# Kernel optimization log

Measured on AMD Instinct MI355X. Metric: run time of the kernel, lower is better.

## Reference

```python
import jax, jax.numpy as jnp
import numpy as np

V, E, H, K, B, T = 50000, 256, 512, 12, 32, 256
START, STOP = 10, 11
NEG = -10000.0
Hd = H // 2


def _lstm(x, h0, c0, Wih, Whh, bih, bhh):
    # x: [T, B, D] -> hidden states [T, B, Hd]; PyTorch gate order i,f,g,o
    def step(carry, xt):
        h, c = carry
        g = xt @ Wih.T + bih + h @ Whh.T + bhh
        i, f, gg, o = jnp.split(g, 4, axis=-1)
        c = jax.nn.sigmoid(f) * c + jax.nn.sigmoid(i) * jnp.tanh(gg)
        h = jax.nn.sigmoid(o) * jnp.tanh(c)
        return (h, c), h
    _, hs = jax.lax.scan(step, (h0, c0), x)
    return hs


def setup_inputs() -> dict:
    key = jax.random.key(0)
    ks = jax.random.split(key, 12)
    inp = {}
    inp["sentence"] = jax.random.randint(ks[0], (B, T), 0, V, dtype=jnp.int32)
    lens = jax.random.randint(ks[1], (B,), 1, T + 1, dtype=jnp.int32)
    inp["seq_lens"] = jnp.sort(lens)[::-1]  # pack_padded requires descending
    emb = jax.random.normal(ks[2], (V, E)) * 0.05
    inp["emb"] = emb.at[0].set(0.0)  # padding_idx=0
    def lw(k):
        a, b, c, d = jax.random.split(k, 4)
        return (jax.random.normal(a, (4 * Hd, E)) * 0.05,
                jax.random.normal(b, (4 * Hd, Hd)) * 0.05,
                jax.random.normal(c, (4 * Hd,)) * 0.05,
                jax.random.normal(d, (4 * Hd,)) * 0.05)
    inp["Wih_f"], inp["Whh_f"], inp["bih_f"], inp["bhh_f"] = lw(ks[3])
    inp["Wih_b"], inp["Whh_b"], inp["bih_b"], inp["bhh_b"] = lw(ks[4])
    inp["h0"] = jax.random.normal(ks[5], (2, B, Hd))  # init_hidden uses randn
    inp["c0"] = jax.random.normal(ks[6], (2, B, Hd))
    inp["W_out"] = jax.random.normal(ks[7], (K, H)) * 0.05
    inp["b_out"] = jax.random.normal(ks[8], (K,)) * 0.05
    trans = jax.random.normal(ks[9], (K, K))
    inp["transitions"] = trans.at[START, :].set(NEG).at[:, STOP].set(NEG)
    return inp


def _features(sentence, seq_lens, emb, Wih_f, Whh_f, bih_f, bhh_f,
              Wih_b, Whh_b, bih_b, bhh_b, h0, c0, W_out, b_out):
    x = emb[sentence]                       # [B,T,E]
    t_idx = jnp.arange(T)
    # forward direction
    hf = _lstm(x.transpose(1, 0, 2), h0[0], c0[0], Wih_f, Whh_f, bih_f, bhh_f)
    hf = hf.transpose(1, 0, 2)              # [B,T,Hd]
    # backward direction: reverse each sequence within its length (packed semantics)
    rev_idx = jnp.where(t_idx[None, :] < seq_lens[:, None],
                        seq_lens[:, None] - 1 - t_idx[None, :], t_idx[None, :])  # [B,T]
    x_rev = jnp.take_along_axis(x, rev_idx[:, :, None], axis=1)
    hb_rev = _lstm(x_rev.transpose(1, 0, 2), h0[1], c0[1], Wih_b, Whh_b, bih_b, bhh_b)
    hb = jnp.take_along_axis(hb_rev.transpose(1, 0, 2), rev_idx[:, :, None], axis=1)
    hcat = jnp.concatenate([hf, hb], axis=-1)  # [B,T,H]
    return hcat @ W_out.T + b_out              # [B,T,K]


def _viterbi(feats, seq_lens, transitions):
    t_idx = jnp.arange(T)
    mask = t_idx[None, :] < seq_lens[:, None]           # [B,T]
    init = jnp.full((B, K), NEG).at[:, START].set(0.0)  # forward_var

    def vstep(fv, inputs):
        feat_t, m_t = inputs                            # [B,K], [B]
        scores = fv[:, None, :] + transitions[None, :, :]   # [B, next, prev]
        bp = jnp.argmax(scores, axis=-1)                # [B,K]
        best = jnp.max(scores, axis=-1) + feat_t
        return jnp.where(m_t[:, None], best, fv), bp

    fv, bps = jax.lax.scan(vstep, init, (feats.transpose(1, 0, 2), mask.T))
    terminal = fv + transitions[STOP][None, :]          # [B,K]
    best_last = jnp.argmax(terminal, axis=-1)           # [B]
    path_scores = jnp.take_along_axis(terminal, best_last[:, None], axis=1)[:, 0]

    def btstep(tag, inputs):
        bp_t, m_t = inputs
        pred_t = jnp.where(m_t, tag, -1)
        prev = jnp.take_along_axis(bp_t, tag[:, None], axis=1)[:, 0]
        return jnp.where(m_t, prev, tag), pred_t

    _, preds_rev = jax.lax.scan(btstep, best_last, (bps[::-1], mask.T[::-1]))
    preds = preds_rev[::-1].transpose(1, 0)             # [B,T], -1 past seq_len
    return path_scores, preds


def reference(sentence, seq_lens, emb, Wih_f, Whh_f, bih_f, bhh_f,
              Wih_b, Whh_b, bih_b, bhh_b, h0, c0, W_out, b_out, transitions):
    feats = _features(sentence, seq_lens, emb, Wih_f, Whh_f, bih_f, bhh_f,
                      Wih_b, Whh_b, bih_b, bhh_b, h0, c0, W_out, b_out)
    scores, preds = _viterbi(feats, seq_lens, transitions)
    return scores, preds
```

## Files before the change

### kernel.cpp

```cpp
#include <hip/hip_runtime.h>
#include <math.h>

#define T_ 256
#define B_ 32
#define E_ 256
#define HD_ 256
#define NG_ 1024
#define K_ 12
#define START_ 10
#define STOP_ 11
#define NEG_ -10000.0f
#define MAGICU 0x40000000u

typedef float f4_t __attribute__((ext_vector_type(4)));

__device__ __forceinline__ float sigf(float x) { return 1.0f / (1.0f + expf(-x)); }

__global__ void tok_gather(const int* __restrict__ sent, const int* __restrict__ lens,
                           int* __restrict__ tokA) {
    int e = blockIdx.x * 256 + threadIdx.x;
    int dir = e >> 13, m = e & 8191, t = m >> 5, b = m & 31;
    int len = lens[b];
    int tt = dir ? (t < len ? len - 1 - t : t) : t;
    tokA[e] = sent[b * T_ + tt];
}

__global__ void whh_tr(const float* __restrict__ Wf, const float* __restrict__ Wb,
                       float* __restrict__ WT) {
    int dir = blockIdx.x >> 8, k = blockIdx.x & 255, u = threadIdx.x;
    const float* W = dir ? Wb : Wf;
    float4 v;
    v.x = W[(0 * HD_ + u) * HD_ + k];
    v.y = W[(1 * HD_ + u) * HD_ + k];
    v.z = W[(2 * HD_ + u) * HD_ + k];
    v.w = W[(3 * HD_ + u) * HD_ + k];
    ((float4*)(WT + ((size_t)dir * 256 + k) * NG_))[u] = v;
}

__global__ void hex_init(float* __restrict__ hex) {
    int i = blockIdx.x * 256 + threadIdx.x;
    float4 m = make_float4(2.0f, 2.0f, 2.0f, 2.0f);
    ((float4*)hex)[i] = m;
}

__global__ __launch_bounds__(256) void in_gemm(
    const float* __restrict__ emb, const int* __restrict__ tokA,
    const float* __restrict__ Wih_f, const float* __restrict__ Wih_b,
    const float* __restrict__ bih_f, const float* __restrict__ bhh_f,
    const float* __restrict__ bih_b, const float* __restrict__ bhh_b,
    float* __restrict__ G) {
    const int dir = blockIdx.z;
    const int n0 = blockIdx.x * 128, m0 = blockIdx.y * 128;
    const float* Wih = dir ? Wih_b : Wih_f;
    const float* bihp = dir ? bih_b : bih_f;
    const float* bhhp = dir ? bhh_b : bhh_f;
    __shared__ float As[8][128];
    __shared__ float Bs[8][128];
    const int tid = threadIdx.x;
    const int rs = tid >> 1, kc = (tid & 1) * 4;
    const int tok = tokA[dir * 8192 + m0 + rs];
    const float* arow = emb + (size_t)tok * E_;
    const int np = n0 + rs;
    const int wrow = ((np & 3) << 8) | (np >> 2);
    const float* brow = Wih + (size_t)wrow * E_;
    const int ty = tid >> 4, tx = tid & 15;

    float acc[8][8];
#pragma unroll
    for (int i = 0; i < 8; ++i)
#pragma unroll
        for (int j = 0; j < 8; ++j) acc[i][j] = 0.f;

    for (int k0 = 0; k0 < E_; k0 += 8) {
        float4 av = *(const float4*)(arow + k0 + kc);
        float4 bv = *(const float4*)(brow + k0 + kc);
        __syncthreads();
        As[kc + 0][rs] = av.x; As[kc + 1][rs] = av.y; As[kc + 2][rs] = av.z; As[kc + 3][rs] = av.w;
        Bs[kc + 0][rs] = bv.x; Bs[kc + 1][rs] = bv.y; Bs[kc + 2][rs] = bv.z; Bs[kc + 3][rs] = bv.w;
        __syncthreads();
#pragma unroll
        for (int k = 0; k < 8; ++k) {
            float4 a0 = *(const float4*)&As[k][ty * 8];
            float4 a1 = *(const float4*)&As[k][ty * 8 + 4];
            float4 b0 = *(const float4*)&Bs[k][tx * 8];
            float4 b1 = *(const float4*)&Bs[k][tx * 8 + 4];
            float af8[8] = {a0.x, a0.y, a0.z, a0.w, a1.x, a1.y, a1.z, a1.w};
            float bf8[8] = {b0.x, b0.y, b0.z, b0.w, b1.x, b1.y, b1.z, b1.w};
#pragma unroll
            for (int i = 0; i < 8; ++i)
#pragma unroll
                for (int j = 0; j < 8; ++j) acc[i][j] += af8[i] * bf8[j];
        }
    }
    float bias[8];
#pragma unroll
    for (int j = 0; j < 8; ++j) {
        int nn = n0 + tx * 8 + j;
        int wr = ((nn & 3) << 8) | (nn >> 2);
        bias[j] = bihp[wr] + bhhp[wr];
    }
#pragma unroll
    for (int i = 0; i < 8; ++i) {
        int m = m0 + ty * 8 + i;
        float* gp = G + ((size_t)dir * 8192 + m) * NG_ + n0 + tx * 8;
        float4 o0 = {acc[i][0] + bias[0], acc[i][1] + bias[1], acc[i][2] + bias[2], acc[i][3] + bias[3]};
        float4 o1 = {acc[i][4] + bias[4], acc[i][5] + bias[5], acc[i][6] + bias[6], acc[i][7] + bias[7]};
        *(float4*)gp = o0;
        *(float4*)(gp + 4) = o1;
    }
}

__global__ __launch_bounds__(512, 2) void lstm_rec8(
    const float* __restrict__ WhhT, const float* __restrict__ G,
    const float* __restrict__ h0, const float* __restrict__ c0,
    const int* __restrict__ lens, float* __restrict__ hex) {
    const int wg = blockIdx.x;
    const int dir = wg >> 5, bt = (wg >> 3) & 3, ut = wg & 7;
    const int tid = threadIdx.x;
    const int wv = tid >> 6, ln = tid & 63;
    const int upair = ln & 15;
    const int kssub = ln >> 4;
    const int ksup = wv >> 1, bh = wv & 1;
    const int ks = ksup * 4 + kssub;
    const int sb = bh * 4 + (ln & 3);
    const int sk = ksup * 64 + (ln >> 2) * 4;
    const int speer = sk >> 5;

    __shared__ float4 hsA4[256];
    __shared__ float4 hsB4[256];
    __shared__ float4 red4[512 * 11];
    __shared__ float4 hT4[64];

    const int Tmax = lens[bt * 8];

    const float4* WT4 = (const float4*)(WhhT + (size_t)dir * 256 * NG_);
    const int gu_e = ut * 32 + upair * 2;
    float4 We[16], Wo[16];
#pragma unroll
    for (int j = 0; j < 16; ++j) {
        We[j] = WT4[(ks * 16 + j) * 256 + gu_e];
        Wo[j] = WT4[(ks * 16 + j) * 256 + gu_e + 1];
    }

    const bool is_act = (ln < 32);
    float c = 0.f;
    float4 gpend = make_float4(0.f, 0.f, 0.f, 0.f);
    const float* Gd = G + (size_t)dir * 8192 * NG_;
    if (is_act) {
        c = c0[(dir * B_ + bt * 8 + wv) * HD_ + ut * 32 + ln];
        gpend = ((const float4*)(Gd + (size_t)(bt * 8 + wv) * NG_))[ut * 32 + ln];
    }

    float* hexg = hex + (size_t)(dir * 4 + bt) * T_ * 2048;
    float4* hsX4 = bh ? hsB4 : hsA4;
    float* hsX = (float*)hsX4;

    f4_t pend;

    for (int t = 0; t < Tmax; ++t) {
        float4 hv;
        if (t == 0) {
            hv = *(const float4*)(h0 + (size_t)(dir * B_ + bt * 8 + sb) * HD_ + sk);
        } else if (speer == ut) {
            hv = hT4[sb * 8 + ((sk & 31) >> 2)];
        } else {
            asm volatile("s_waitcnt vmcnt(0)" ::: "memory");
            hv.x = pend.x; hv.y = pend.y; hv.z = pend.z; hv.w = pend.w;
            if (__float_as_uint(hv.x) == MAGICU || __float_as_uint(hv.y) == MAGICU ||
                __float_as_uint(hv.z) == MAGICU || __float_as_uint(hv.w) == MAGICU) {
                const float* src = hexg + (size_t)(t - 1) * 2048 + sb * 256 + sk;
                int it = 0;
                for (;;) {
                    __builtin_amdgcn_s_sleep(1);
                    float a0 = __hip_atomic_load(src + 0, __ATOMIC_RELAXED, __HIP_MEMORY_SCOPE_AGENT);
                    float a1 = __hip_atomic_load(src + 1, __ATOMIC_RELAXED, __HIP_MEMORY_SCOPE_AGENT);
                    float a2 = __hip_atomic_load(src + 2, __ATOMIC_RELAXED, __HIP_MEMORY_SCOPE_AGENT);
                    float a3 = __hip_atomic_load(src + 3, __ATOMIC_RELAXED, __HIP_MEMORY_SCOPE_AGENT);
                    if (!(__float_as_uint(a0) == MAGICU || __float_as_uint(a1) == MAGICU ||
                          __float_as_uint(a2) == MAGICU || __float_as_uint(a3) == MAGICU)) {
                        hv = make_float4(a0, a1, a2, a3); break;
                    }
                    if (++it > (1 << 22)) break;
                }
            }
        }
        hsX[(sk + 0) * 4 + (ln & 3)] = hv.x;
        hsX[(sk + 1) * 4 + (ln & 3)] = hv.y;
        hsX[(sk + 2) * 4 + (ln & 3)] = hv.z;
        hsX[(sk + 3) * 4 + (ln & 3)] = hv.w;
        asm volatile("s_waitcnt lgkmcnt(0)" ::: "memory");

        float4 ae0 = {0,0,0,0}, ae1 = {0,0,0,0}, ae2 = {0,0,0,0}, ae3 = {0,0,0,0};
        float4 ao0 = {0,0,0,0}, ao1 = {0,0,0,0}, ao2 = {0,0,0,0}, ao3 = {0,0,0,0};
#pragma unroll
        for (int j = 0; j < 16; ++j) {
            float4 h4 = hsX4[ks * 16 + j];
            float4 we = We[j], wo = Wo[j];
            ae0.x += we.x*h4.x; ae0.y += we.y*h4.x; ae0.z += we.z*h4.x; ae0.w += we.w*h4.x;
            ae1.x += we.x*h4.y; ae1.y += we.y*h4.y; ae1.z += we.z*h4.y; ae1.w += we.w*h4.y;
            ae2.x += we.x*h4.z; ae2.y += we.y*h4.z; ae2.z += we.z*h4.z; ae2.w += we.w*h4.z;
            ae3.x += we.x*h4.w; ae3.y += we.y*h4.w; ae3.z += we.z*h4.w; ae3.w += we.w*h4.w;
            ao0.x += wo.x*h4.x; ao0.y += wo.y*h4.x; ao0.z += wo.z*h4.x; ao0.w += wo.w*h4.x;
            ao1.x += wo.x*h4.y; ao1.y += wo.y*h4.y; ao1.z += wo.z*h4.y; ao1.w += wo.w*h4.y;
            ao2.x += wo.x*h4.z; ao2.y += wo.y*h4.z; ao2.z += wo.z*h4.z; ao2.w += wo.w*h4.z;
            ao3.x += wo.x*h4.w; ao3.y += wo.y*h4.w; ao3.z += wo.z*h4.w; ao3.w += wo.w*h4.w;
        }
        {
            float4* r = &red4[((wv * 4 + kssub) * 16 + upair) * 11 + kssub];
            r[0] = ae0; r[1] = ae1; r[2] = ae2; r[3] = ae3;
            r[4] = ao0; r[5] = ao1; r[6] = ao2; r[7] = ao3;
        }
        asm volatile("s_waitcnt lgkmcnt(0)\n\ts_barrier" ::: "memory");

        if (is_act) {
            const int b = wv, u = ln;
            const int bhv = b >> 2, bq = b & 3, up = u >> 1, par = u & 1;
            float si = gpend.x, sf = gpend.y, sg = gpend.z, so = gpend.w;
#pragma unroll
            for (int kq = 0; kq < 4; ++kq)
#pragma unroll
                for (int kr = 0; kr < 4; ++kr) {
                    float4 p = red4[(((kq * 2 + bhv) * 4 + kr) * 16 + up) * 11 + kr + par * 4 + bq];
                    si += p.x; sf += p.y; sg += p.z; so += p.w;
                }
            c = sigf(sf) * c + sigf(si) * tanhf(sg);
            float h = sigf(so) * tanhf(c);
            ((float*)hT4)[b * 32 + u] = h;
            float* dst = hexg + (size_t)t * 2048 + b * 256 + ut * 32 + u;
            asm volatile("global_store_dword %0, %1, off sc0 sc1" :: "v"(dst), "v"(h) : "memory");
            if (t + 1 < Tmax)
                gpend = ((const float4*)(Gd + ((size_t)(t + 1) * B_ + bt * 8 + b) * NG_))[ut * 32 + u];
        }
        if (t + 1 < Tmax && speer != ut) {
            const float* nsrc = hexg + (size_t)t * 2048 + sb * 256 + sk;
            asm volatile("global_load_dwordx4 %0, %1, off sc0 sc1"
                         : "=v"(pend) : "v"(nsrc) : "memory");
        }
        asm volatile("s_waitcnt lgkmcnt(0)\n\ts_barrier" ::: "memory");
    }
}

__global__ void feat_k(const float* __restrict__ hex, const int* __restrict__ lens,
                       const float* __restrict__ Wout, const float* __restrict__ bout,
                       float* __restrict__ feats) {
    int tid = threadIdx.x;
    int pl = tid / 12, k = tid % 12;
    int p = blockIdx.x * 16 + pl;
    int b = p >> 8, t = p & 255;
    int len = lens[b];
    int tr = t < len ? len - 1 - t : t;
    const float4* hf = (const float4*)(hex + ((size_t)(b >> 3) * T_ + t) * 2048 + (b & 7) * 256);
    const float4* hb = (const float4*)(hex + ((size_t)(4 + (b >> 3)) * T_ + tr) * 2048 + (b & 7) * 256);
    const float4* w0 = (const float4*)(Wout + (size_t)k * 512);
    const float4* w1 = (const float4*)(Wout + (size_t)k * 512 + 256);
    float acc = bout[k];
#pragma unroll 4
    for (int j = 0; j < 64; ++j) {
        float4 h4 = hf[j], v4 = w0[j];
        acc += h4.x * v4.x + h4.y * v4.y + h4.z * v4.z + h4.w * v4.w;
    }
#pragma unroll 4
    for (int j = 0; j < 64; ++j) {
        float4 h4 = hb[j], v4 = w1[j];
        acc += h4.x * v4.x + h4.y * v4.y + h4.z * v4.z + h4.w * v4.w;
    }
    feats[(size_t)p * K_ + k] = acc;
}

__global__ __launch_bounds__(512) void viterbi_k(
    const float* __restrict__ feats, const float* __restrict__ trans,
    const int* __restrict__ lens, float* __restrict__ out) {
    __shared__ float fv[2][B_][16];
    __shared__ float tl[K_][16];
    __shared__ unsigned char bp[T_][B_][6];
    __shared__ int best_last[B_];
    int tid = threadIdx.x;
    int b = tid >> 4, lane = tid & 15;
    if (tid < K_ * K_) tl[tid / 12][tid % 12] = trans[tid];
    if (lane < K_) fv[0][b][lane] = (lane == START_) ? 0.f : NEG_;
    __syncthreads();
    int len = lens[b];
    int pp = 0;
    float f_cur = 0.f;
    if (lane < K_) f_cur = feats[(size_t)b * T_ * K_ + lane];
    for (int t = 0; t < T_; ++t) {
        float f_nxt = 0.f;
        if (t + 1 < T_ && lane < K_) f_nxt = feats[((size_t)b * T_ + t + 1) * K_ + lane];
        if (lane < K_) {
            float best = fv[pp][b][0] + tl[lane][0];
            int argp = 0;
#pragma unroll
            for (int p = 1; p < K_; ++p) {
                float v = fv[pp][b][p] + tl[lane][p];
                if (v > best) { best = v; argp = p; }
            }
            float nb = best + f_cur;
            fv[pp ^ 1][b][lane] = (t < len) ? nb : fv[pp][b][lane];
            int other = __shfl_xor(argp, 1);
            if ((lane & 1) == 0) bp[t][b][lane >> 1] = (unsigned char)(argp | (other << 4));
        }
        __syncthreads();
        pp ^= 1;
        f_cur = f_nxt;
    }
    if (lane == 0) {
        float best = fv[pp][b][0] + tl[STOP_][0];
        int bl = 0;
#pragma unroll
        for (int p = 1; p < K_; ++p) {
            float v = fv[pp][b][p] + tl[STOP_][p];
            if (v > best) { best = v; bl = p; }
        }
        out[b] = best;
        best_last[b] = bl;
    }
    __syncthreads();
    if (lane == 0) {
        int tag = best_last[b];
        for (int t = T_ - 1; t >= 0; --t) {
            int m = (t < len);
            out[B_ + b * T_ + t] = (float)(m ? tag : -1);
            if (m) tag = (bp[t][b][tag >> 1] >> ((tag & 1) * 4)) & 15;
        }
    }
}

extern "C" void kernel_launch(void* const* d_in, const int* in_sizes, int n_in,
                              void* d_out, int out_size, void* d_ws, size_t ws_size,
                              hipStream_t stream) {
    const int*   sent  = (const int*)d_in[0];
    const int*   lens  = (const int*)d_in[1];
    const float* emb   = (const float*)d_in[2];
    const float* Wih_f = (const float*)d_in[3];
    const float* Whh_f = (const float*)d_in[4];
    const float* bih_f = (const float*)d_in[5];
    const float* bhh_f = (const float*)d_in[6];
    const float* Wih_b = (const float*)d_in[7];
    const float* Whh_b = (const float*)d_in[8];
    const float* bih_b = (const float*)d_in[9];
    const float* bhh_b = (const float*)d_in[10];
    const float* h0    = (const float*)d_in[11];
    const float* c0    = (const float*)d_in[12];
    const float* Wout  = (const float*)d_in[13];
    const float* bout  = (const float*)d_in[14];
    const float* trans = (const float*)d_in[15];
    float* out = (float*)d_out;

    char* ws = (char*)d_ws;
    int*   tokA  = (int*)ws;
    float* WhhT  = (float*)(ws + 65536);
    float* G     = (float*)(ws + 2162688);
    float* feats = (float*)(ws + 69271552);
    float* hex   = (float*)(ws + 69664768);

    tok_gather<<<64, 256, 0, stream>>>(sent, lens, tokA);
    whh_tr<<<512, 256, 0, stream>>>(Whh_f, Whh_b, WhhT);
    hex_init<<<4096, 256, 0, stream>>>(hex);
    in_gemm<<<dim3(8, 64, 2), 256, 0, stream>>>(emb, tokA, Wih_f, Wih_b,
                                                bih_f, bhh_f, bih_b, bhh_b, G);
    lstm_rec8<<<64, 512, 0, stream>>>(WhhT, G, h0, c0, lens, hex);
    feat_k<<<512, 192, 0, stream>>>(hex, lens, Wout, bout, feats);
    viterbi_k<<<1, 512, 0, stream>>>(feats, trans, lens, out);
}
```

Measured before the change: 1.132 ms.

## Remap recurrence blocks across XCDs and relax coherence bits on peer hidden-state loads

The block-to-work mapping changes so the 8 blocks that share a direction and batch tile (exchanging h each step) get consecutive-by-8 block IDs. With round-robin dispatch these likely land on the same XCD and share its L2. Peer h loads drop the sc1 bit, and the spin loop uses a vector load that only bypasses further every fourth try. This aims to cut cross-die coherence latency on each step's h exchange, but it relies on co-location and could read stale data or spin longer if blocks land on different XCDs.

```diff
diff --git a/kernel.cpp b/kernel.cpp
--- a/kernel.cpp
+++ b/kernel.cpp
@@ -110,12 +110,13 @@
     }
 }
 
-__global__ __launch_bounds__(512, 2) void lstm_rec8(
+__global__ __launch_bounds__(512, 2) void lstm_rec9(
     const float* __restrict__ WhhT, const float* __restrict__ G,
     const float* __restrict__ h0, const float* __restrict__ c0,
     const int* __restrict__ lens, float* __restrict__ hex) {
-    const int wg = blockIdx.x;
-    const int dir = wg >> 5, bt = (wg >> 3) & 3, ut = wg & 7;
+    const int g = blockIdx.x & 7;
+    const int ut = blockIdx.x >> 3;
+    const int dir = g >> 2, bt = g & 3;
     const int tid = threadIdx.x;
     const int wv = tid >> 6, ln = tid & 63;
     const int upair = ln & 15;
@@ -152,8 +153,6 @@
     }
 
     float* hexg = hex + (size_t)(dir * 4 + bt) * T_ * 2048;
-    float4* hsX4 = bh ? hsB4 : hsA4;
-    float* hsX = (float*)hsX4;
 
     f4_t pend;
 
@@ -172,24 +171,30 @@
                 int it = 0;
                 for (;;) {
                     __builtin_amdgcn_s_sleep(1);
-                    float a0 = __hip_atomic_load(src + 0, __ATOMIC_RELAXED, __HIP_MEMORY_SCOPE_AGENT);
-                    float a1 = __hip_atomic_load(src + 1, __ATOMIC_RELAXED, __HIP_MEMORY_SCOPE_AGENT);
-                    float a2 = __hip_atomic_load(src + 2, __ATOMIC_RELAXED, __HIP_MEMORY_SCOPE_AGENT);
-                    float a3 = __hip_atomic_load(src + 3, __ATOMIC_RELAXED, __HIP_MEMORY_SCOPE_AGENT);
-                    if (!(__float_as_uint(a0) == MAGICU || __float_as_uint(a1) == MAGICU ||
-                          __float_as_uint(a2) == MAGICU || __float_as_uint(a3) == MAGICU)) {
-                        hv = make_float4(a0, a1, a2, a3); break;
+                    f4_t r;
+                    if ((it & 3) == 3) {
+                        asm volatile("global_load_dwordx4 %0, %1, off sc0 sc1\n\ts_waitcnt vmcnt(0)"
+                                     : "=v"(r) : "v"(src) : "memory");
+                    } else {
+                        asm volatile("global_load_dwordx4 %0, %1, off sc0\n\ts_waitcnt vmcnt(0)"
+                                     : "=v"(r) : "v"(src) : "memory");
+                    }
+                    if (!(__float_as_uint(r.x) == MAGICU || __float_as_uint(r.y) == MAGICU ||
+                          __float_as_uint(r.z) == MAGICU || __float_as_uint(r.w) == MAGICU)) {
+                        hv.x = r.x; hv.y = r.y; hv.z = r.z; hv.w = r.w; break;
                     }
                     if (++it > (1 << 22)) break;
                 }
             }
         }
+        float* hsX = (float*)(bh ? hsB4 : hsA4);
         hsX[(sk + 0) * 4 + (ln & 3)] = hv.x;
         hsX[(sk + 1) * 4 + (ln & 3)] = hv.y;
         hsX[(sk + 2) * 4 + (ln & 3)] = hv.z;
         hsX[(sk + 3) * 4 + (ln & 3)] = hv.w;
         asm volatile("s_waitcnt lgkmcnt(0)" ::: "memory");
 
+        const float4* hsX4 = bh ? hsB4 : hsA4;
         float4 ae0 = {0,0,0,0}, ae1 = {0,0,0,0}, ae2 = {0,0,0,0}, ae3 = {0,0,0,0};
         float4 ao0 = {0,0,0,0}, ao1 = {0,0,0,0}, ao2 = {0,0,0,0}, ao3 = {0,0,0,0};
 #pragma unroll
@@ -233,7 +238,7 @@
         }
         if (t + 1 < Tmax && speer != ut) {
             const float* nsrc = hexg + (size_t)t * 2048 + sb * 256 + sk;
-            asm volatile("global_load_dwordx4 %0, %1, off sc0 sc1"
+            asm volatile("global_load_dwordx4 %0, %1, off sc0"
                          : "=v"(pend) : "v"(nsrc) : "memory");
         }
         asm volatile("s_waitcnt lgkmcnt(0)\n\ts_barrier" ::: "memory");
@@ -358,7 +363,7 @@
     hex_init<<<4096, 256, 0, stream>>>(hex);
     in_gemm<<<dim3(8, 64, 2), 256, 0, stream>>>(emb, tokA, Wih_f, Wih_b,
                                                 bih_f, bhh_f, bih_b, bhh_b, G);
-    lstm_rec8<<<64, 512, 0, stream>>>(WhhT, G, h0, c0, lens, hex);
+    lstm_rec9<<<64, 512, 0, stream>>>(WhhT, G, h0, c0, lens, hex);
     feat_k<<<512, 192, 0, stream>>>(hex, lens, Wout, bout, feats);
     viterbi_k<<<1, 512, 0, stream>>>(feats, trans, lens, out);
 }
```

Measured after the change: 1.260 ms. +11.3%, slower.
